# Kernel optimization log

Hardware: AMD Instinct MI355X
Metric: run time of the kernel (lower is better)

## Reference

```python
import jax, jax.numpy as jnp
import numpy as np

B, S, D, H = 2, 2048, 1024, 16
HD = D // H
NEG = -10000000000.0

def setup_inputs() -> dict:
    key = jax.random.key(0)
    ks = jax.random.split(key, 9)
    s = 1.0 / np.sqrt(D)
    return {
        "x": jax.random.normal(ks[0], (B, S, D), dtype=jnp.float32),
        "Wq": jax.random.uniform(ks[1], (D, D), jnp.float32, -s, s),
        "bq": jax.random.uniform(ks[2], (D,), jnp.float32, -s, s),
        "Wk": jax.random.uniform(ks[3], (D, D), jnp.float32, -s, s),
        "bk": jax.random.uniform(ks[4], (D,), jnp.float32, -s, s),
        "Wv": jax.random.uniform(ks[5], (D, D), jnp.float32, -s, s),
        "bv": jax.random.uniform(ks[6], (D,), jnp.float32, -s, s),
        "Wo": jax.random.uniform(ks[7], (D, D), jnp.float32, -s, s),
        "bo": jax.random.uniform(ks[8], (D,), jnp.float32, -s, s),
    }

def reference(x, Wq, bq, Wk, bk, Wv, bv, Wo, bo):
    b, s, _ = x.shape
    def split_heads(t):
        return t.reshape(b, s, H, HD).transpose(0, 2, 1, 3)  # [b,h,s,hd]
    Q = split_heads(x @ Wq + bq)
    K = split_heads(x @ Wk + bk)
    V = split_heads(x @ Wv + bv)
    scores = jnp.einsum('bhqd,bhkd->bhqk', Q, K) / jnp.sqrt(jnp.float32(HD))
    causal = jnp.tril(jnp.ones((s, s), dtype=bool))
    scores = jnp.where(causal[None, None], scores, NEG)
    attn = jax.nn.softmax(scores, axis=-1)
    ctx = jnp.einsum('bhqk,bhkd->bhqd', attn, V)
    ctx = ctx.transpose(0, 2, 1, 3).reshape(b, s, D)
    return ctx @ Wo + bo
```

## Files before the change

### kernel.cpp

```cpp
#include <hip/hip_runtime.h>
#include <hip/hip_bf16.h>

#define BB 2
#define SS 2048
#define DD 1024
#define HH 16
#define HD 64
#define MM (BB*SS)

typedef __attribute__((ext_vector_type(8))) short bf16x8;
typedef __attribute__((ext_vector_type(4))) float f32x4;

#define QSCALE 0.18033688f

static __device__ __forceinline__ unsigned short f2bf(float f) {
    unsigned int u = __builtin_bit_cast(unsigned int, f);
    u += 0x7fffu + ((u >> 16) & 1u);
    return (unsigned short)(u >> 16);
}

static __device__ __forceinline__ void gload16(const unsigned short* g, unsigned short* l) {
    __builtin_amdgcn_global_load_lds(
        (const __attribute__((address_space(1))) unsigned int*)g,
        (__attribute__((address_space(3))) unsigned int*)l, 16, 0, 0);
}

__global__ __launch_bounds__(256) void prep_kernel(const float* __restrict__ x,
                                                   const float* __restrict__ W0,
                                                   const float* __restrict__ W1,
                                                   const float* __restrict__ W2,
                                                   const float* __restrict__ W3,
                                                   unsigned short* __restrict__ xb,
                                                   unsigned short* __restrict__ Wt)
{
    const int t = threadIdx.x;
    const int bid = blockIdx.x;
    if (bid < 2048) {
        const size_t i = ((size_t)bid * 256 + t) * 8;
        float4 a = *(const float4*)(x + i);
        float4 b = *(const float4*)(x + i + 4);
        union { unsigned short u[8]; bf16x8 v; } pk;
        pk.u[0] = f2bf(a.x); pk.u[1] = f2bf(a.y); pk.u[2] = f2bf(a.z); pk.u[3] = f2bf(a.w);
        pk.u[4] = f2bf(b.x); pk.u[5] = f2bf(b.y); pk.u[6] = f2bf(b.z); pk.u[7] = f2bf(b.w);
        *(bf16x8*)(xb + i) = pk.v;
        return;
    }
    __shared__ unsigned short Ts[64][72];
    const int wsel = (bid - 2048) >> 8;
    const int rem  = (bid - 2048) & 255;
    const float* W = wsel == 0 ? W0 : wsel == 1 ? W1 : wsel == 2 ? W2 : W3;
    unsigned short* out = Wt + (size_t)wsel * DD * DD;
    const int n0 = (rem & 15) * 64, k0 = (rem >> 4) * 64;
#pragma unroll
    for (int i = 0; i < 4; ++i) {
        const int r = (t >> 4) + i * 16;
        const int c = (t & 15) * 4;
        float4 v = *(const float4*)(W + (size_t)(k0 + r) * DD + n0 + c);
        Ts[c + 0][r] = f2bf(v.x); Ts[c + 1][r] = f2bf(v.y);
        Ts[c + 2][r] = f2bf(v.z); Ts[c + 3][r] = f2bf(v.w);
    }
    __syncthreads();
#pragma unroll
    for (int j = 0; j < 2; ++j) {
        const int ch = j * 256 + t;
        const int rn = ch >> 3, ck = (ch & 7) * 8;
        bf16x8 v = *(const bf16x8*)&Ts[rn][ck];
        *(bf16x8*)(out + (size_t)(n0 + rn) * DD + k0 + ck) = v;
    }
}

__global__ __launch_bounds__(256) void gemm_mfma(const unsigned short* __restrict__ A,
                                                 const unsigned short* __restrict__ Bt,
                                                 const float* __restrict__ bias0,
                                                 const float* __restrict__ bias1,
                                                 const float* __restrict__ bias2,
                                                 unsigned short* __restrict__ Qb,
                                                 unsigned short* __restrict__ Kb,
                                                 unsigned short* __restrict__ Vb,
                                                 float* __restrict__ outf,
                                                 int mode)
{
    __shared__ unsigned short As[128 * 32];
    __shared__ unsigned short Bs[128 * 32];

    const int t = threadIdx.x;
    const int w = t >> 6, l = t & 63;
    const int lane16 = l & 15, quad = l >> 4;
    const int m0 = blockIdx.x * 128, n0 = blockIdx.y * 128;
    const int wm = (w & 1) * 64, wn = (w >> 1) * 64;

    f32x4 acc[4][4] = {};

    const int r0 = t >> 2,         g0 = (t & 3) ^ ((r0 >> 1) & 3);
    const int r1 = (256 + t) >> 2, g1 = (t & 3) ^ ((r1 >> 1) & 3);

    const int fs = quad ^ ((lane16 >> 1) & 3);

    for (int k0 = 0; k0 < DD; k0 += 32) {
        __syncthreads();
        gload16(A  + (size_t)(m0 + r0) * DD + k0 + g0 * 8, As + t * 8);
        gload16(A  + (size_t)(m0 + r1) * DD + k0 + g1 * 8, As + (256 + t) * 8);
        gload16(Bt + (size_t)(n0 + r0) * DD + k0 + g0 * 8, Bs + t * 8);
        gload16(Bt + (size_t)(n0 + r1) * DD + k0 + g1 * 8, Bs + (256 + t) * 8);
        __syncthreads();

        bf16x8 af[4], bfr[4];
#pragma unroll
        for (int mt = 0; mt < 4; ++mt)
            af[mt] = *(const bf16x8*)&As[((wm + mt * 16 + lane16) * 4 + fs) * 8];
#pragma unroll
        for (int nt = 0; nt < 4; ++nt)
            bfr[nt] = *(const bf16x8*)&Bs[((wn + nt * 16 + lane16) * 4 + fs) * 8];
#pragma unroll
        for (int mt = 0; mt < 4; ++mt)
#pragma unroll
            for (int nt = 0; nt < 4; ++nt)
                acc[mt][nt] = __builtin_amdgcn_mfma_f32_16x16x32_bf16(af[mt], bfr[nt], acc[mt][nt], 0, 0, 0);
    }

    if (mode == 0) {
        const int which = n0 >> 10;
        const float* bias = which == 0 ? bias0 : which == 1 ? bias1 : bias2;
#pragma unroll
        for (int nt = 0; nt < 4; ++nt) {
            const int gcol = n0 + wn + nt * 16 + lane16;
            const int cd = gcol & 1023;
            const float bv = bias[cd];
            const int h_ = cd >> 6, d = cd & 63;
            if (which == 2) {
#pragma unroll
                for (int mt = 0; mt < 4; ++mt) {
                    const int row0 = m0 + wm + mt * 16 + quad * 4;
                    const int b_ = row0 >> 11, s0 = row0 & 2047;
                    union { unsigned short u[4]; uint2 v; } pk;
#pragma unroll
                    for (int r = 0; r < 4; ++r) pk.u[r] = f2bf(acc[mt][nt][r] + bv);
                    *(uint2*)(Vb + ((size_t)(b_ * HH + h_) * HD + d) * SS + s0) = pk.v;
                }
            } else {
                unsigned short* dst3 = which == 0 ? Qb : Kb;
                const float sc_ = which == 0 ? QSCALE : 1.0f;
#pragma unroll
                for (int mt = 0; mt < 4; ++mt)
#pragma unroll
                    for (int r = 0; r < 4; ++r) {
                        const int row = m0 + wm + mt * 16 + quad * 4 + r;
                        const int b_ = row >> 11, s_ = row & 2047;
                        dst3[(((size_t)(b_ * HH + h_) * SS + s_) * HD) + d] =
                            f2bf((acc[mt][nt][r] + bv) * sc_);
                    }
            }
        }
    } else {
#pragma unroll
        for (int nt = 0; nt < 4; ++nt) {
            const int gcol = n0 + wn + nt * 16 + lane16;
            const float bv = bias0[gcol];
#pragma unroll
            for (int mt = 0; mt < 4; ++mt)
#pragma unroll
                for (int r = 0; r < 4; ++r) {
                    const int row = m0 + wm + mt * 16 + quad * 4 + r;
                    outf[(size_t)row * DD + gcol] = acc[mt][nt][r] + bv;
                }
        }
    }
}

__global__ __launch_bounds__(512) void attn_mfma(const unsigned short* __restrict__ Q,
                                                 const unsigned short* __restrict__ K,
                                                 const unsigned short* __restrict__ V,
                                                 unsigned short* __restrict__ ctx)
{
    __shared__ unsigned short Ks[2][4096];
    __shared__ unsigned short Vs[2][4096];
    __shared__ unsigned short Ps[8][1280];

    const int t = threadIdx.x;
    const int w = t >> 6, l = t & 63;
    const int lane16 = l & 15, quad = l >> 4;
    const int bid = blockIdx.x;
    const int halfg = bid >> 8, idx = bid & 255;
    const int qb_ = idx >> 5;
    const int qblk = halfg ? qb_ : 15 - qb_;
    const int hb = idx & 31;
    const int h = hb & 15, b = hb >> 4;
    const int q0 = qblk * 128;
    const size_t bh = (size_t)(b * HH + h) * SS;
    const unsigned short* Vg = V + (size_t)(b * HH + h) * HD * SS;

    const int wrow0 = q0 + w * 16;
    bf16x8 qf0 = *(const bf16x8*)(Q + (bh + wrow0 + lane16) * HD + quad * 8);
    bf16x8 qf1 = *(const bf16x8*)(Q + (bh + wrow0 + lane16) * HD + 32 + quad * 8);

    f32x4 Oc[4] = {};
    float lpart[4] = {};

    const int ntiles = 2 * qblk + 2;
    const int sr = t >> 3;
    const int sg = (t & 7) ^ (sr & 7);

    {
        gload16(K  + (bh + sr) * HD + sg * 8, &Ks[0][t * 8]);
        gload16(Vg + (size_t)sr * SS + sg * 8, &Vs[0][t * 8]);
    }

    for (int kt = 0; kt < ntiles; ++kt) {
        __syncthreads();
        if (kt + 1 < ntiles) {
            const int k1 = (kt + 1) * 64;
            const int bi = (kt + 1) & 1;
            gload16(K  + (bh + k1 + sr) * HD + sg * 8, &Ks[bi][t * 8]);
            gload16(Vg + (size_t)sr * SS + k1 + sg * 8, &Vs[bi][t * 8]);
        }
        const int k0 = kt * 64;
        if (k0 > wrow0 + 15) continue;
        const unsigned short* Kt = Ks[kt & 1];
        const unsigned short* Vt = Vs[kt & 1];

        f32x4 sc[4] = {};
#pragma unroll
        for (int nt = 0; nt < 4; ++nt) {
            const int row = nt * 16 + lane16;
            bf16x8 k0f = *(const bf16x8*)&Kt[(row * 8 + (quad ^ (row & 7))) * 8];
            bf16x8 k1f = *(const bf16x8*)&Kt[(row * 8 + ((4 + quad) ^ (row & 7))) * 8];
            sc[nt] = __builtin_amdgcn_mfma_f32_16x16x32_bf16(qf0, k0f, sc[nt], 0, 0, 0);
            sc[nt] = __builtin_amdgcn_mfma_f32_16x16x32_bf16(qf1, k1f, sc[nt], 0, 0, 0);
        }

        float pr[4][4];
        if (k0 + 63 > wrow0) {
#pragma unroll
            for (int r = 0; r < 4; ++r) {
                const int row = wrow0 + quad * 4 + r;
#pragma unroll
                for (int nt = 0; nt < 4; ++nt)
                    if (k0 + nt * 16 + lane16 > row) sc[nt][r] = -1e30f;
            }
        }
#pragma unroll
        for (int nt = 0; nt < 4; ++nt)
#pragma unroll
            for (int r = 0; r < 4; ++r) pr[nt][r] = __builtin_amdgcn_exp2f(sc[nt][r]);
#pragma unroll
        for (int r = 0; r < 4; ++r)
            lpart[r] += (pr[0][r] + pr[1][r]) + (pr[2][r] + pr[3][r]);

        unsigned short* Pw = Ps[w];
#pragma unroll
        for (int nt = 0; nt < 4; ++nt) {
            const int plane = (nt >> 1) * 640, colin = (nt & 1) * 16 + lane16;
#pragma unroll
            for (int r = 0; r < 4; ++r)
                Pw[plane + (quad * 4 + r) * 40 + colin] = f2bf(pr[nt][r]);
        }
        bf16x8 pf0 = *(const bf16x8*)&Pw[lane16 * 40 + quad * 8];
        bf16x8 pf1 = *(const bf16x8*)&Pw[640 + lane16 * 40 + quad * 8];

#pragma unroll
        for (int dt = 0; dt < 4; ++dt) {
            const int drow = dt * 16 + lane16;
            bf16x8 v0 = *(const bf16x8*)&Vt[(drow * 8 + (quad ^ (drow & 7))) * 8];
            bf16x8 v1 = *(const bf16x8*)&Vt[(drow * 8 + ((4 + quad) ^ (drow & 7))) * 8];
            Oc[dt] = __builtin_amdgcn_mfma_f32_16x16x32_bf16(pf0, v0, Oc[dt], 0, 0, 0);
            Oc[dt] = __builtin_amdgcn_mfma_f32_16x16x32_bf16(pf1, v1, Oc[dt], 0, 0, 0);
        }
    }

#pragma unroll
    for (int off = 1; off < 16; off <<= 1)
#pragma unroll
        for (int r = 0; r < 4; ++r) lpart[r] += __shfl_xor(lpart[r], off);

#pragma unroll
    for (int r = 0; r < 4; ++r) {
        const float inv = 1.f / lpart[r];
        const int row = wrow0 + quad * 4 + r;
        unsigned short* dst = ctx + ((size_t)(b * SS) + row) * DD + h * HD + lane16;
#pragma unroll
        for (int dt = 0; dt < 4; ++dt) dst[dt * 16] = f2bf(Oc[dt][r] * inv);
    }
}

extern "C" void kernel_launch(void* const* d_in, const int* in_sizes, int n_in,
                              void* d_out, int out_size, void* d_ws, size_t ws_size,
                              hipStream_t stream) {
    const float* x  = (const float*)d_in[0];
    const float* Wq = (const float*)d_in[1];
    const float* bq = (const float*)d_in[2];
    const float* Wk = (const float*)d_in[3];
    const float* bk = (const float*)d_in[4];
    const float* Wv = (const float*)d_in[5];
    const float* bv = (const float*)d_in[6];
    const float* Wo = (const float*)d_in[7];
    const float* bo = (const float*)d_in[8];
    float* out = (float*)d_out;

    unsigned short* xb  = (unsigned short*)d_ws;
    unsigned short* Wt  = xb  + (size_t)MM * DD;
    unsigned short* Qb  = Wt  + (size_t)4 * DD * DD;
    unsigned short* Kb  = Qb  + (size_t)MM * DD;
    unsigned short* Vb  = Kb  + (size_t)MM * DD;
    unsigned short* ctxb = Vb + (size_t)MM * DD;

    prep_kernel<<<2048 + 1024, 256, 0, stream>>>(x, Wq, Wk, Wv, Wo, xb, Wt);

    gemm_mfma<<<dim3(MM / 128, 3072 / 128), 256, 0, stream>>>(
        xb, Wt, bq, bk, bv, Qb, Kb, Vb, nullptr, 0);

    attn_mfma<<<(SS / 128) * HH * BB, 512, 0, stream>>>(Qb, Kb, Vb, ctxb);

    gemm_mfma<<<dim3(MM / 128, DD / 128), 256, 0, stream>>>(
        ctxb, Wt + (size_t)3 * DD * DD, bo, nullptr, nullptr,
        nullptr, nullptr, nullptr, out, 1);
}
```

Baseline: 200.0 us.

## Store Q transposed like V and drop LDS swizzle in projection GEMM

The projection GEMM now writes Q in a head-dim-major (transposed) layout with packed 8-byte stores, matching how V is stored, instead of scattered 2-byte row-major stores. The attention kernel gathers each Q fragment with strided 2-byte global loads from the transposed layout. Separately, the XOR swizzle on the GEMM's LDS tiles is removed in favour of a plain row-major layout. Removing the swizzle likely brings back LDS bank conflicts on the fragment reads, and the Q gathers in attention are uncoalesced, though they happen only once per block.

```diff
diff --git a/kernel.cpp b/kernel.cpp
--- a/kernel.cpp
+++ b/kernel.cpp
@@ -91,26 +91,25 @@
 
     f32x4 acc[4][4] = {};
 
-    const int r0 = t >> 2,         g0 = (t & 3) ^ ((r0 >> 1) & 3);
-    const int r1 = (256 + t) >> 2, g1 = (t & 3) ^ ((r1 >> 1) & 3);
-
-    const int fs = quad ^ ((lane16 >> 1) & 3);
+    const int c0 = t, c1 = 256 + t;
+    const int r0 = c0 >> 2, kc0 = (c0 & 3) * 8;
+    const int r1 = c1 >> 2, kc1 = (c1 & 3) * 8;
 
     for (int k0 = 0; k0 < DD; k0 += 32) {
         __syncthreads();
-        gload16(A  + (size_t)(m0 + r0) * DD + k0 + g0 * 8, As + t * 8);
-        gload16(A  + (size_t)(m0 + r1) * DD + k0 + g1 * 8, As + (256 + t) * 8);
-        gload16(Bt + (size_t)(n0 + r0) * DD + k0 + g0 * 8, Bs + t * 8);
-        gload16(Bt + (size_t)(n0 + r1) * DD + k0 + g1 * 8, Bs + (256 + t) * 8);
+        gload16(A  + (size_t)(m0 + r0) * DD + k0 + kc0, As + c0 * 8);
+        gload16(A  + (size_t)(m0 + r1) * DD + k0 + kc1, As + c1 * 8);
+        gload16(Bt + (size_t)(n0 + r0) * DD + k0 + kc0, Bs + c0 * 8);
+        gload16(Bt + (size_t)(n0 + r1) * DD + k0 + kc1, Bs + c1 * 8);
         __syncthreads();
 
         bf16x8 af[4], bfr[4];
 #pragma unroll
         for (int mt = 0; mt < 4; ++mt)
-            af[mt] = *(const bf16x8*)&As[((wm + mt * 16 + lane16) * 4 + fs) * 8];
+            af[mt] = *(const bf16x8*)&As[(wm + mt * 16 + lane16) * 32 + quad * 8];
 #pragma unroll
         for (int nt = 0; nt < 4; ++nt)
-            bfr[nt] = *(const bf16x8*)&Bs[((wn + nt * 16 + lane16) * 4 + fs) * 8];
+            bfr[nt] = *(const bf16x8*)&Bs[(wn + nt * 16 + lane16) * 32 + quad * 8];
 #pragma unroll
         for (int mt = 0; mt < 4; ++mt)
 #pragma unroll
@@ -127,27 +126,27 @@
             const int cd = gcol & 1023;
             const float bv = bias[cd];
             const int h_ = cd >> 6, d = cd & 63;
-            if (which == 2) {
+            if (which != 1) {
+                unsigned short* dstT = which == 0 ? Qb : Vb;
+                const float sc_ = which == 0 ? QSCALE : 1.0f;
 #pragma unroll
                 for (int mt = 0; mt < 4; ++mt) {
                     const int row0 = m0 + wm + mt * 16 + quad * 4;
                     const int b_ = row0 >> 11, s0 = row0 & 2047;
                     union { unsigned short u[4]; uint2 v; } pk;
 #pragma unroll
-                    for (int r = 0; r < 4; ++r) pk.u[r] = f2bf(acc[mt][nt][r] + bv);
-                    *(uint2*)(Vb + ((size_t)(b_ * HH + h_) * HD + d) * SS + s0) = pk.v;
+                    for (int r = 0; r < 4; ++r) pk.u[r] = f2bf((acc[mt][nt][r] + bv) * sc_);
+                    *(uint2*)(dstT + ((size_t)(b_ * HH + h_) * HD + d) * SS + s0) = pk.v;
                 }
             } else {
-                unsigned short* dst3 = which == 0 ? Qb : Kb;
-                const float sc_ = which == 0 ? QSCALE : 1.0f;
 #pragma unroll
                 for (int mt = 0; mt < 4; ++mt)
 #pragma unroll
                     for (int r = 0; r < 4; ++r) {
                         const int row = m0 + wm + mt * 16 + quad * 4 + r;
                         const int b_ = row >> 11, s_ = row & 2047;
-                        dst3[(((size_t)(b_ * HH + h_) * SS + s_) * HD) + d] =
-                            f2bf((acc[mt][nt][r] + bv) * sc_);
+                        Kb[(((size_t)(b_ * HH + h_) * SS + s_) * HD) + d] =
+                            f2bf(acc[mt][nt][r] + bv);
                     }
             }
         }
@@ -188,10 +187,16 @@
     const int q0 = qblk * 128;
     const size_t bh = (size_t)(b * HH + h) * SS;
     const unsigned short* Vg = V + (size_t)(b * HH + h) * HD * SS;
+    const unsigned short* Qg = Q + (size_t)(b * HH + h) * HD * SS;
 
     const int wrow0 = q0 + w * 16;
-    bf16x8 qf0 = *(const bf16x8*)(Q + (bh + wrow0 + lane16) * HD + quad * 8);
-    bf16x8 qf1 = *(const bf16x8*)(Q + (bh + wrow0 + lane16) * HD + 32 + quad * 8);
+    union { unsigned short u[8]; bf16x8 v; } q0u, q1u;
+#pragma unroll
+    for (int j = 0; j < 8; ++j) {
+        q0u.u[j] = Qg[(size_t)(quad * 8 + j) * SS + wrow0 + lane16];
+        q1u.u[j] = Qg[(size_t)(32 + quad * 8 + j) * SS + wrow0 + lane16];
+    }
+    const bf16x8 qf0 = q0u.v, qf1 = q1u.v;
 
     f32x4 Oc[4] = {};
     float lpart[4] = {};
```

Measured after the change: 204.8 us. 2.4% more time.
